# Kernel optimization log

Hardware: AMD Instinct MI355X
Metric: run time of the kernel (lower is better)

## Reference

```python
import jax, jax.numpy as jnp
import numpy as np

B, S, HLEN, VLEN, HID = 32, 2048, 1024, 1024, 1024


def setup_inputs() -> dict:
    key = jax.random.key(0)
    ks = jax.random.split(key, 6)
    scale_W = 1.0 / np.sqrt(HLEN)
    scale_U = 1.0 / np.sqrt(VLEN)
    scale_w = 1.0 / np.sqrt(HID)
    return {
        "h": jax.random.normal(ks[0], (B, HLEN), dtype=jnp.float32),
        "V": jax.random.normal(ks[1], (B, S, VLEN), dtype=jnp.float32),
        "W_w": jax.random.normal(ks[2], (HID, HLEN), dtype=jnp.float32) * scale_W,
        "W_b": jax.random.normal(ks[3], (HID,), dtype=jnp.float32) * scale_W,
        "U_w": jax.random.normal(ks[4], (HID, VLEN), dtype=jnp.float32) * scale_U,
        "w_w": jax.random.normal(ks[5], (HID,), dtype=jnp.float32) * scale_w,
    }


def reference(h, V, W_w, W_b, U_w, w_w):
    # e = w^T tanh(W h + U V^T + b); beta = softmax(e); out = sum_s beta_s V_s
    h_proj = h @ W_w.T + W_b                      # [B, HID]
    V_proj = jnp.einsum('bsv,dv->bsd', V, U_w)    # [B, S, HID]
    e = jnp.einsum('bsd,d->bs', jnp.tanh(h_proj[:, None, :] + V_proj), w_w)  # [B, S]
    beta = jax.nn.softmax(e, axis=1)              # [B, S]
    return jnp.einsum('bs,bsv->bv', beta, V)      # [B, VLEN]
```

## Files before the change

kernel.cpp:

```cpp
#include <hip/hip_runtime.h>

constexpr int B_   = 32;
constexpr int S_   = 2048;
constexpr int HID_ = 1024;
constexpr int VL_  = 1024;

typedef __attribute__((ext_vector_type(4))) float  f32x4;
typedef __attribute__((ext_vector_type(4))) short  s16x4;
typedef __attribute__((ext_vector_type(8))) short  s16x8;

__device__ __forceinline__ short f2bf(float f) {
    union { float f; unsigned u; } v; v.f = f;
    unsigned r = v.u + 0x7fffu + ((v.u >> 16) & 1u);
    return (short)(r >> 16);
}

__device__ __forceinline__ float bf2f(short s) {
    union { unsigned u; float f; } v;
    v.u = ((unsigned)(unsigned short)s) << 16;
    return v.f;
}

__device__ __forceinline__ float fast_tanh(float x) {
    float e2 = __expf(2.0f * x);
    return 1.0f - 2.0f / (e2 + 1.0f);
}

__device__ __forceinline__ void async_cp16(const void* g, void* l) {
    __builtin_amdgcn_global_load_lds(
        (const __attribute__((address_space(1))) unsigned int*)g,
        (__attribute__((address_space(3))) unsigned int*)l,
        16, 0, 0);
}

__global__ __launch_bounds__(256) void hproj_kernel(const float* __restrict__ h,
                                                    const float* __restrict__ Ww,
                                                    const float* __restrict__ Wb,
                                                    float* __restrict__ hp) {
    int tid = threadIdx.x;
    int wave = tid >> 6, lane = tid & 63;
    int d = blockIdx.x * 4 + wave;
    const float* wr = Ww + (size_t)d * HID_;
    float4 wreg[4];
#pragma unroll
    for (int i = 0; i < 4; i++) wreg[i] = *(const float4*)(wr + i * 256 + lane * 4);
    float bias = Wb[d];
    for (int b = 0; b < B_; b++) {
        const float* hr = h + (size_t)b * HID_;
        float acc = 0.0f;
#pragma unroll
        for (int i = 0; i < 4; i++) {
            float4 x = *(const float4*)(hr + i * 256 + lane * 4);
            acc += wreg[i].x * x.x + wreg[i].y * x.y + wreg[i].z * x.z + wreg[i].w * x.w;
        }
#pragma unroll
        for (int o = 32; o; o >>= 1) acc += __shfl_xor(acc, o);
        if (lane == 0) hp[(size_t)b * HID_ + d] = acc + bias;
    }
}

__global__ __launch_bounds__(256) void cvt_kernel(const float* __restrict__ src,
                                                  short* __restrict__ dst, size_t n4) {
    size_t i = (size_t)blockIdx.x * blockDim.x + threadIdx.x;
    size_t stride = (size_t)gridDim.x * blockDim.x;
    for (; i < n4; i += stride) {
        float4 x = ((const float4*)src)[i];
        s16x4 y;
        y.x = f2bf(x.x); y.y = f2bf(x.y); y.z = f2bf(x.z); y.w = f2bf(x.w);
        ((s16x4*)dst)[i] = y;
    }
}

__global__ __launch_bounds__(256) void e_kernel_bf16(const short* __restrict__ Vm,
                                                     const short* __restrict__ Um,
                                                     const float* __restrict__ hp,
                                                     const float* __restrict__ ww,
                                                     float* __restrict__ epart) {
    __shared__ short As[128][32];
    __shared__ short Bs[128][32];
    __shared__ float ebuf[2][128];

    int tid = threadIdx.x;
    int dh = blockIdx.x;
    int s0 = blockIdx.y * 128;
    int b  = blockIdx.z;
    int wave = tid >> 6, lane = tid & 63;
    int wm = wave >> 1, wn = wave & 1;
    int col = lane & 15, quad = lane >> 4;

    int r0 = 32 * wave + (lane >> 2);
    int kc = (lane & 3) * 8;
    const short* gAb = Vm + ((size_t)b * S_ + s0 + r0) * VL_ + kc;
    short* lA0 = &As[32 * wave][0];
    short* lA1 = &As[32 * wave + 16][0];
    short* lB0 = &Bs[32 * wave][0];
    short* lB1 = &Bs[32 * wave + 16][0];

    float ep[4][4];
#pragma unroll
    for (int i = 0; i < 4; i++)
#pragma unroll
        for (int j = 0; j < 4; j++) ep[i][j] = 0.0f;

    for (int dt = dh * 4; dt < dh * 4 + 4; dt++) {
        int d0 = dt * 128;
        const short* gA0 = gAb;
        const short* gA1 = gAb + 16 * (size_t)VL_;
        const short* gB0 = Um + ((size_t)d0 + r0) * VL_ + kc;
        const short* gB1 = gB0 + 16 * (size_t)VL_;

        f32x4 zero = {0.f, 0.f, 0.f, 0.f};
        f32x4 acc[4][4];
#pragma unroll
        for (int i = 0; i < 4; i++)
#pragma unroll
            for (int j = 0; j < 4; j++) acc[i][j] = zero;

        for (int k0 = 0; k0 < VL_; k0 += 32) {
            async_cp16(gA0, lA0);
            async_cp16(gA1, lA1);
            async_cp16(gB0, lB0);
            async_cp16(gB1, lB1);
            gA0 += 32; gA1 += 32; gB0 += 32; gB1 += 32;
            __syncthreads();

            s16x8 a8[4], b8[4];
#pragma unroll
            for (int tm = 0; tm < 4; tm++)
                a8[tm] = *(const s16x8*)&As[wm * 64 + tm * 16 + col][quad * 8];
#pragma unroll
            for (int tn = 0; tn < 4; tn++)
                b8[tn] = *(const s16x8*)&Bs[wn * 64 + tn * 16 + col][quad * 8];
#pragma unroll
            for (int tm = 0; tm < 4; tm++)
#pragma unroll
                for (int tn = 0; tn < 4; tn++)
                    acc[tm][tn] = __builtin_amdgcn_mfma_f32_16x16x32_bf16(
                        a8[tm], b8[tn], acc[tm][tn], 0, 0, 0);
            __syncthreads();
        }

        float wv[4], hv[4];
#pragma unroll
        for (int tn = 0; tn < 4; tn++) {
            int d = d0 + wn * 64 + tn * 16 + col;
            wv[tn] = ww[d];
            hv[tn] = hp[(size_t)b * HID_ + d];
        }
#pragma unroll
        for (int tm = 0; tm < 4; tm++)
#pragma unroll
            for (int reg = 0; reg < 4; reg++) {
#pragma unroll
                for (int tn = 0; tn < 4; tn++)
                    ep[tm][reg] += wv[tn] * fast_tanh(hv[tn] + acc[tm][tn][reg]);
            }
    }

#pragma unroll
    for (int tm = 0; tm < 4; tm++)
#pragma unroll
        for (int reg = 0; reg < 4; reg++) {
            float p = ep[tm][reg];
            p += __shfl_xor(p, 1);
            p += __shfl_xor(p, 2);
            p += __shfl_xor(p, 4);
            p += __shfl_xor(p, 8);
            if (col == 0)
                ebuf[wn][wm * 64 + tm * 16 + quad * 4 + reg] = p;
        }
    __syncthreads();
    if (tid < 128)
        epart[((size_t)dh * B_ + b) * S_ + s0 + tid] = ebuf[0][tid] + ebuf[1][tid];
}

__global__ __launch_bounds__(256) void e_kernel_f32(const float* __restrict__ Vm,
                                                    const float* __restrict__ Um,
                                                    const float* __restrict__ hp,
                                                    const float* __restrict__ ww,
                                                    float* __restrict__ e) {
    __shared__ short As[128][40];
    __shared__ short Bs[128][40];
    int tid = threadIdx.x;
    int b  = blockIdx.z;
    int d0 = blockIdx.x * 128;
    int s0 = blockIdx.y * 128;
    int wave = tid >> 6, lane = tid & 63;
    int wm = wave >> 1, wn = wave & 1;
    int col = lane & 15, quad = lane >> 4;

    f32x4 zero = {0.f, 0.f, 0.f, 0.f};
    f32x4 acc[4][4];
#pragma unroll
    for (int i = 0; i < 4; i++)
#pragma unroll
        for (int j = 0; j < 4; j++) acc[i][j] = zero;

    const float* Abase = Vm + ((size_t)b * S_ + s0) * (size_t)VL_;
    const float* Bbase = Um + (size_t)d0 * (size_t)VL_;

    for (int k0 = 0; k0 < VL_; k0 += 32) {
        int k4 = tid & 7, rb = tid >> 3;
#pragma unroll
        for (int i = 0; i < 4; i++) {
            int r = rb + 32 * i;
            float4 x = *(const float4*)(Abase + (size_t)r * VL_ + k0 + k4 * 4);
            s16x4 ya; ya.x = f2bf(x.x); ya.y = f2bf(x.y); ya.z = f2bf(x.z); ya.w = f2bf(x.w);
            *(s16x4*)&As[r][k4 * 4] = ya;
            float4 y = *(const float4*)(Bbase + (size_t)r * VL_ + k0 + k4 * 4);
            s16x4 yb; yb.x = f2bf(y.x); yb.y = f2bf(y.y); yb.z = f2bf(y.z); yb.w = f2bf(y.w);
            *(s16x4*)&Bs[r][k4 * 4] = yb;
        }
        __syncthreads();
        s16x8 a8[4], b8[4];
#pragma unroll
        for (int tm = 0; tm < 4; tm++)
            a8[tm] = *(const s16x8*)&As[wm * 64 + tm * 16 + col][quad * 8];
#pragma unroll
        for (int tn = 0; tn < 4; tn++)
            b8[tn] = *(const s16x8*)&Bs[wn * 64 + tn * 16 + col][quad * 8];
#pragma unroll
        for (int tm = 0; tm < 4; tm++)
#pragma unroll
            for (int tn = 0; tn < 4; tn++)
                acc[tm][tn] = __builtin_amdgcn_mfma_f32_16x16x32_bf16(
                    a8[tm], b8[tn], acc[tm][tn], 0, 0, 0);
        __syncthreads();
    }

    float wv[4], hv[4];
#pragma unroll
    for (int tn = 0; tn < 4; tn++) {
        int d = d0 + wn * 64 + tn * 16 + col;
        wv[tn] = ww[d];
        hv[tn] = hp[(size_t)b * HID_ + d];
    }
#pragma unroll
    for (int tm = 0; tm < 4; tm++) {
#pragma unroll
        for (int reg = 0; reg < 4; reg++) {
            float p = 0.0f;
#pragma unroll
            for (int tn = 0; tn < 4; tn++)
                p += wv[tn] * fast_tanh(hv[tn] + acc[tm][tn][reg]);
            p += __shfl_xor(p, 1);
            p += __shfl_xor(p, 2);
            p += __shfl_xor(p, 4);
            p += __shfl_xor(p, 8);
            if (col == 0) {
                int s = s0 + wm * 64 + tm * 16 + quad * 4 + reg;
                atomicAdd(&e[(size_t)b * S_ + s], p);
            }
        }
    }
}

__global__ __launch_bounds__(256) void softmax_kernel(const float* __restrict__ epart,
                                                      float* __restrict__ beta,
                                                      int nparts) {
    int b = blockIdx.x, tid = threadIdx.x;
    const float* r0 = epart + (size_t)b * S_;
    const float* r1 = epart + ((size_t)B_ + b) * S_;
    float v[8];
    float m = -1e30f;
#pragma unroll
    for (int i = 0; i < 8; i++) {
        int idx = tid + i * 256;
        v[i] = r0[idx] + (nparts > 1 ? r1[idx] : 0.0f);
        m = fmaxf(m, v[i]);
    }
#pragma unroll
    for (int o = 32; o; o >>= 1) m = fmaxf(m, __shfl_xor(m, o));
    __shared__ float rm[4], rs[4];
    int wave = tid >> 6, lane = tid & 63;
    if (lane == 0) rm[wave] = m;
    __syncthreads();
    m = fmaxf(fmaxf(rm[0], rm[1]), fmaxf(rm[2], rm[3]));
    float s = 0.0f;
#pragma unroll
    for (int i = 0; i < 8; i++) { v[i] = __expf(v[i] - m); s += v[i]; }
#pragma unroll
    for (int o = 32; o; o >>= 1) s += __shfl_xor(s, o);
    if (lane == 0) rs[wave] = s;
    __syncthreads();
    s = rs[0] + rs[1] + rs[2] + rs[3];
    float inv = 1.0f / s;
#pragma unroll
    for (int i = 0; i < 8; i++) beta[(size_t)b * S_ + tid + i * 256] = v[i] * inv;
}

__global__ __launch_bounds__(256) void out_kernel_bf16(const float* __restrict__ beta,
                                                       const short* __restrict__ Vb16,
                                                       float* __restrict__ opart) {
    int b = blockIdx.x, sc = blockIdx.y;
    int v4 = threadIdx.x;
    const short* Vp = Vb16 + ((size_t)b * S_ + (size_t)sc * 128) * VL_;
    const float* bb = beta + (size_t)b * S_ + (size_t)sc * 128;
    float ax = 0.f, ay = 0.f, az = 0.f, aw = 0.f;
    for (int s = 0; s < 128; s++) {
        float w = bb[s];
        s16x4 x = *(const s16x4*)(Vp + (size_t)s * VL_ + v4 * 4);
        ax += w * bf2f(x.x); ay += w * bf2f(x.y);
        az += w * bf2f(x.z); aw += w * bf2f(x.w);
    }
    float4 r = {ax, ay, az, aw};
    *(float4*)(opart + (((size_t)b * 16 + sc) * VL_) + v4 * 4) = r;
}

__global__ __launch_bounds__(256) void out_reduce_kernel(const float* __restrict__ opart,
                                                         float* __restrict__ out) {
    int b = blockIdx.x, v4 = threadIdx.x;
    float4 a = {0.f, 0.f, 0.f, 0.f};
    const float* base = opart + (size_t)b * 16 * VL_;
#pragma unroll
    for (int sc = 0; sc < 16; sc++) {
        float4 x = *(const float4*)(base + (size_t)sc * VL_ + v4 * 4);
        a.x += x.x; a.y += x.y; a.z += x.z; a.w += x.w;
    }
    *(float4*)(out + (size_t)b * VL_ + v4 * 4) = a;
}

__global__ __launch_bounds__(256) void out_kernel_f32(const float* __restrict__ beta,
                                                      const float* __restrict__ V,
                                                      float* __restrict__ out) {
    int b = blockIdx.x, sc = blockIdx.y;
    int v4 = threadIdx.x;
    const float* Vb = V + ((size_t)b * S_ + (size_t)sc * 128) * VL_;
    const float* bb = beta + (size_t)b * S_ + (size_t)sc * 128;
    float ax = 0.f, ay = 0.f, az = 0.f, aw = 0.f;
    for (int s = 0; s < 128; s++) {
        float w = bb[s];
        float4 x = *(const float4*)(Vb + (size_t)s * VL_ + v4 * 4);
        ax += w * x.x; ay += w * x.y; az += w * x.z; aw += w * x.w;
    }
    float* o = out + (size_t)b * VL_ + v4 * 4;
    atomicAdd(o + 0, ax);
    atomicAdd(o + 1, ay);
    atomicAdd(o + 2, az);
    atomicAdd(o + 3, aw);
}

extern "C" void kernel_launch(void* const* d_in, const int* in_sizes, int n_in,
                              void* d_out, int out_size, void* d_ws, size_t ws_size,
                              hipStream_t stream) {
    const float* h  = (const float*)d_in[0];
    const float* V  = (const float*)d_in[1];
    const float* Ww = (const float*)d_in[2];
    const float* Wb = (const float*)d_in[3];
    const float* Uw = (const float*)d_in[4];
    const float* ww = (const float*)d_in[5];
    float* out = (float*)d_out;

    char* ws = (char*)d_ws;
    float* hp    = (float*)ws;
    float* epart = (float*)(ws + 131072);
    float* beta  = (float*)(ws + 131072 + 524288);
    float* opart = (float*)(ws + 131072 + 524288 + 262144);
    size_t fixed = 131072 + 524288 + 262144 + 2097152;
    short* Vb16 = (short*)(ws + fixed);
    short* Ub16 = Vb16 + (size_t)B_ * S_ * VL_;
    size_t need = fixed + ((size_t)B_ * S_ * VL_ + (size_t)HID_ * VL_) * 2;
    bool bf16path = (ws_size >= need);

    hproj_kernel<<<dim3(HID_ / 4), 256, 0, stream>>>(h, Ww, Wb, hp);

    if (bf16path) {
        cvt_kernel<<<4096, 256, 0, stream>>>(V, Vb16, (size_t)B_ * S_ * VL_ / 4);
        cvt_kernel<<<256, 256, 0, stream>>>(Uw, Ub16, (size_t)HID_ * VL_ / 4);
        e_kernel_bf16<<<dim3(2, S_ / 128, B_), 256, 0, stream>>>(Vb16, Ub16, hp, ww, epart);
        softmax_kernel<<<B_, 256, 0, stream>>>(epart, beta, 2);
        out_kernel_bf16<<<dim3(B_, S_ / 128), 256, 0, stream>>>(beta, Vb16, opart);
        out_reduce_kernel<<<B_, 256, 0, stream>>>(opart, out);
    } else {
        hipMemsetAsync(epart, 0, (size_t)B_ * S_ * 4, stream);
        hipMemsetAsync(out, 0, (size_t)out_size * 4, stream);
        e_kernel_f32<<<dim3(HID_ / 128, S_ / 128, B_), 256, 0, stream>>>(
            V, Uw, hp, ww, epart);
        softmax_kernel<<<B_, 256, 0, stream>>>(epart, beta, 1);
        out_kernel_f32<<<dim3(B_, S_ / 128), 256, 0, stream>>>(beta, V, out);
    }
}
```

Measured before the change: 663.0 us.

## Rewrite bf16 score GEMM as 256x256 double-buffered 8-wave pipelined kernel

Replaces the 128x128 single-buffered e-kernel with a 512-thread kernel that computes a 256-row S tile across the full hidden dimension. It uses double-buffered LDS with XOR-swizzled chunks to avoid bank conflicts, issues prefetch of the next K tile between MFMA phases, and raises wave priority around MFMA groups. Because each block covers all of HID, the split-D partial sums are gone and softmax reads a single partial. The cost is a larger accumulator footprint, more LDS per block, and a smaller grid of 256 blocks, which may limit occupancy.

```diff
diff --git a/kernel.cpp b/kernel.cpp
--- a/kernel.cpp
+++ b/kernel.cpp
@@ -71,107 +71,138 @@
     }
 }
 
-__global__ __launch_bounds__(256) void e_kernel_bf16(const short* __restrict__ Vm,
-                                                     const short* __restrict__ Um,
-                                                     const float* __restrict__ hp,
-                                                     const float* __restrict__ ww,
-                                                     float* __restrict__ epart) {
-    __shared__ short As[128][32];
-    __shared__ short Bs[128][32];
-    __shared__ float ebuf[2][128];
-
-    int tid = threadIdx.x;
-    int dh = blockIdx.x;
-    int s0 = blockIdx.y * 128;
-    int b  = blockIdx.z;
-    int wave = tid >> 6, lane = tid & 63;
-    int wm = wave >> 1, wn = wave & 1;
-    int col = lane & 15, quad = lane >> 4;
-
-    int r0 = 32 * wave + (lane >> 2);
-    int kc = (lane & 3) * 8;
-    const short* gAb = Vm + ((size_t)b * S_ + s0 + r0) * VL_ + kc;
-    short* lA0 = &As[32 * wave][0];
-    short* lA1 = &As[32 * wave + 16][0];
-    short* lB0 = &Bs[32 * wave][0];
-    short* lB1 = &Bs[32 * wave + 16][0];
-
-    float ep[4][4];
-#pragma unroll
-    for (int i = 0; i < 4; i++)
+constexpr int BM_E = 256;
+constexpr int BK_E = 64;
+constexpr int NT_E = VL_ / BK_E;
+
+__global__ __launch_bounds__(512, 2) void e_kernel_8ph(const short* __restrict__ Vm,
+                                                       const short* __restrict__ Um,
+                                                       const float* __restrict__ hp,
+                                                       const float* __restrict__ ww,
+                                                       float* __restrict__ e) {
+    __shared__ short Al[2][BM_E][BK_E];
+    __shared__ short Bl[2][BM_E][BK_E];
+
+    const int tid  = threadIdx.x;
+    const int wave = tid >> 6, lane = tid & 63;
+    const int wm = wave >> 2, wn = wave & 3;
+    const int col = lane & 15, quad = lane >> 4;
+    const int rx  = col & 7;
+    const int s0 = blockIdx.x * BM_E;
+    const int b  = blockIdx.y;
+
+    const int srow   = lane >> 3;
+    const int schunk = (lane & 7) ^ srow;
+
+    const short* gA = Vm + ((size_t)b * S_ + s0 + wave * 8 + srow) * VL_ + schunk * 8;
+    const short* gB = Um + (size_t)(wave * 8 + srow) * VL_ + schunk * 8;
+
+    float ep[8][4];
+#pragma unroll
+    for (int i = 0; i < 8; i++)
 #pragma unroll
         for (int j = 0; j < 4; j++) ep[i][j] = 0.0f;
 
-    for (int dt = dh * 4; dt < dh * 4 + 4; dt++) {
-        int d0 = dt * 128;
-        const short* gA0 = gAb;
-        const short* gA1 = gAb + 16 * (size_t)VL_;
-        const short* gB0 = Um + ((size_t)d0 + r0) * VL_ + kc;
-        const short* gB1 = gB0 + 16 * (size_t)VL_;
-
+    for (int dt = 0; dt < 4; ++dt) {
+        const int d0 = dt * 256;
+
+        f32x4 acc[8][4];
         f32x4 zero = {0.f, 0.f, 0.f, 0.f};
-        f32x4 acc[4][4];
-#pragma unroll
-        for (int i = 0; i < 4; i++)
+#pragma unroll
+        for (int i = 0; i < 8; i++)
 #pragma unroll
             for (int j = 0; j < 4; j++) acc[i][j] = zero;
 
-        for (int k0 = 0; k0 < VL_; k0 += 32) {
-            async_cp16(gA0, lA0);
-            async_cp16(gA1, lA1);
-            async_cp16(gB0, lB0);
-            async_cp16(gB1, lB1);
-            gA0 += 32; gA1 += 32; gB0 += 32; gB1 += 32;
-            __syncthreads();
-
-            s16x8 a8[4], b8[4];
-#pragma unroll
-            for (int tm = 0; tm < 4; tm++)
-                a8[tm] = *(const s16x8*)&As[wm * 64 + tm * 16 + col][quad * 8];
-#pragma unroll
-            for (int tn = 0; tn < 4; tn++)
-                b8[tn] = *(const s16x8*)&Bs[wn * 64 + tn * 16 + col][quad * 8];
-#pragma unroll
-            for (int tm = 0; tm < 4; tm++)
-#pragma unroll
-                for (int tn = 0; tn < 4; tn++)
-                    acc[tm][tn] = __builtin_amdgcn_mfma_f32_16x16x32_bf16(
-                        a8[tm], b8[tn], acc[tm][tn], 0, 0, 0);
-            __syncthreads();
+#pragma unroll
+        for (int r = 0; r < 4; ++r) {
+            async_cp16(gA + (size_t)(r * 64) * VL_, &Al[0][r * 64 + wave * 8][0]);
+            async_cp16(gB + ((size_t)(d0 + r * 64)) * VL_, &Bl[0][r * 64 + wave * 8][0]);
+        }
+        asm volatile("s_waitcnt vmcnt(0)" ::: "memory");
+        __builtin_amdgcn_s_barrier();
+
+        for (int t = 0; t < NT_E; ++t) {
+            const int c = t & 1;
+            s16x8 b8[4][2];
+            s16x8 a8[2][2];
+#pragma unroll
+            for (int p = 0; p < 4; ++p) {
+#pragma unroll
+                for (int i = 0; i < 2; ++i)
+#pragma unroll
+                    for (int kk = 0; kk < 2; ++kk)
+                        a8[i][kk] = *(const s16x8*)&Al[c][wm * 128 + (2 * p + i) * 16 + col]
+                                                        [((((kk << 2) | quad) ^ rx) << 3)];
+                if (p == 0) {
+#pragma unroll
+                    for (int tn = 0; tn < 4; ++tn)
+#pragma unroll
+                        for (int kk = 0; kk < 2; ++kk)
+                            b8[tn][kk] = *(const s16x8*)&Bl[c][wn * 64 + tn * 16 + col]
+                                                             [((((kk << 2) | quad) ^ rx) << 3)];
+                }
+                if (p == 0 && t + 1 < NT_E) {
+                    const short* g = gA + (size_t)(t + 1) * BK_E;
+#pragma unroll
+                    for (int r = 0; r < 4; ++r)
+                        async_cp16(g + (size_t)(r * 64) * VL_, &Al[c ^ 1][r * 64 + wave * 8][0]);
+                }
+                if (p == 1 && t + 1 < NT_E) {
+                    const short* g = gB + (size_t)d0 * VL_ + (size_t)(t + 1) * BK_E;
+#pragma unroll
+                    for (int r = 0; r < 4; ++r)
+                        async_cp16(g + (size_t)(r * 64) * VL_, &Bl[c ^ 1][r * 64 + wave * 8][0]);
+                }
+                __builtin_amdgcn_s_barrier();
+                __builtin_amdgcn_s_setprio(1);
+#pragma unroll
+                for (int kk = 0; kk < 2; ++kk)
+#pragma unroll
+                    for (int i = 0; i < 2; ++i)
+#pragma unroll
+                        for (int tn = 0; tn < 4; ++tn)
+                            acc[2 * p + i][tn] = __builtin_amdgcn_mfma_f32_16x16x32_bf16(
+                                a8[i][kk], b8[tn][kk], acc[2 * p + i][tn], 0, 0, 0);
+                __builtin_amdgcn_s_setprio(0);
+                if (p == 3)
+                    asm volatile("s_waitcnt vmcnt(0)" ::: "memory");
+                __builtin_amdgcn_s_barrier();
+            }
         }
 
         float wv[4], hv[4];
 #pragma unroll
-        for (int tn = 0; tn < 4; tn++) {
+        for (int tn = 0; tn < 4; ++tn) {
             int d = d0 + wn * 64 + tn * 16 + col;
             wv[tn] = ww[d];
             hv[tn] = hp[(size_t)b * HID_ + d];
         }
 #pragma unroll
-        for (int tm = 0; tm < 4; tm++)
-#pragma unroll
-            for (int reg = 0; reg < 4; reg++) {
-#pragma unroll
-                for (int tn = 0; tn < 4; tn++)
+        for (int tm = 0; tm < 8; ++tm)
+#pragma unroll
+            for (int reg = 0; reg < 4; ++reg)
+#pragma unroll
+                for (int tn = 0; tn < 4; ++tn)
                     ep[tm][reg] += wv[tn] * fast_tanh(hv[tn] + acc[tm][tn][reg]);
-            }
-    }
-
-#pragma unroll
-    for (int tm = 0; tm < 4; tm++)
-#pragma unroll
-        for (int reg = 0; reg < 4; reg++) {
+    }
+
+    float* eb = (float*)&Al[0][0][0];
+#pragma unroll
+    for (int tm = 0; tm < 8; ++tm)
+#pragma unroll
+        for (int reg = 0; reg < 4; ++reg) {
             float p = ep[tm][reg];
             p += __shfl_xor(p, 1);
             p += __shfl_xor(p, 2);
             p += __shfl_xor(p, 4);
             p += __shfl_xor(p, 8);
             if (col == 0)
-                ebuf[wn][wm * 64 + tm * 16 + quad * 4 + reg] = p;
+                eb[wn * 256 + wm * 128 + tm * 16 + quad * 4 + reg] = p;
         }
     __syncthreads();
-    if (tid < 128)
-        epart[((size_t)dh * B_ + b) * S_ + s0 + tid] = ebuf[0][tid] + ebuf[1][tid];
+    if (tid < 256)
+        e[(size_t)b * S_ + s0 + tid] =
+            eb[tid] + eb[256 + tid] + eb[512 + tid] + eb[768 + tid];
 }
 
 __global__ __launch_bounds__(256) void e_kernel_f32(const float* __restrict__ Vm,
@@ -367,8 +398,8 @@
     if (bf16path) {
         cvt_kernel<<<4096, 256, 0, stream>>>(V, Vb16, (size_t)B_ * S_ * VL_ / 4);
         cvt_kernel<<<256, 256, 0, stream>>>(Uw, Ub16, (size_t)HID_ * VL_ / 4);
-        e_kernel_bf16<<<dim3(2, S_ / 128, B_), 256, 0, stream>>>(Vb16, Ub16, hp, ww, epart);
-        softmax_kernel<<<B_, 256, 0, stream>>>(epart, beta, 2);
+        e_kernel_8ph<<<dim3(S_ / BM_E, B_), 512, 0, stream>>>(Vb16, Ub16, hp, ww, epart);
+        softmax_kernel<<<B_, 256, 0, stream>>>(epart, beta, 1);
         out_kernel_bf16<<<dim3(B_, S_ / 128), 256, 0, stream>>>(beta, Vb16, opart);
         out_reduce_kernel<<<B_, 256, 0, stream>>>(opart, out);
     } else {
```

Measured after the change: 593.6 us. -10.5%, faster.
